# Optimization experiments

Hardware: AMD Instinct MI355X
Metric: run time of the kernel (lower is better)

## Reference

```python
import jax, jax.numpy as jnp
import numpy as np

T = 2048           # tokens (single prefill sequence)
HIDDEN = 2048
H = 16             # num heads
D_NOPE = 128
D_ROPE = 64
D_V = 128
KV_LORA = 512
EPS = 1e-6
ROPE_THETA = 10000.0


def setup_inputs() -> dict:
    key = jax.random.key(0)
    ks = jax.random.split(key, 7)
    s = 0.02
    return {
        "positions": jnp.arange(T, dtype=jnp.int64) if jax.config.jax_enable_x64 else jnp.arange(T, dtype=jnp.int32),
        "hidden_states": jax.random.normal(ks[0], (T, HIDDEN), dtype=jnp.float32),
        "w_q": jax.random.normal(ks[1], (HIDDEN, H * (D_NOPE + D_ROPE)), dtype=jnp.float32) * s,
        "w_kv_a": jax.random.normal(ks[2], (HIDDEN, KV_LORA + D_ROPE), dtype=jnp.float32) * s,
        "kv_a_ln_w": jax.random.uniform(ks[3], (KV_LORA,), dtype=jnp.float32, minval=0.5, maxval=1.5),
        "w_kv_b": jax.random.normal(ks[4], (KV_LORA, H * (D_NOPE + D_V)), dtype=jnp.float32) * s,
        "w_o": jax.random.normal(ks[5], (H * D_V, HIDDEN), dtype=jnp.float32) * s,
    }


def _rms_norm(x, w):
    var = jnp.mean(jnp.square(x), axis=-1, keepdims=True)
    return x * jax.lax.rsqrt(var + EPS) * w


def _rope_nonneox(x, positions):
    # x: [..., D_ROPE], GPT-J (interleaved) style rotation
    inv_freq = 1.0 / (ROPE_THETA ** (jnp.arange(0, D_ROPE, 2, dtype=jnp.float32) / D_ROPE))
    freqs = positions.astype(jnp.float32)[:, None] * inv_freq  # [T, D_ROPE//2]
    cos, sin = jnp.cos(freqs), jnp.sin(freqs)
    # broadcast over head dim if present
    while cos.ndim < x.ndim:
        cos, sin = cos[:, None], sin[:, None]
    x1, x2 = x[..., 0::2], x[..., 1::2]
    o1 = x1 * cos - x2 * sin
    o2 = x2 * cos + x1 * sin
    return jnp.stack([o1, o2], axis=-1).reshape(x.shape)


def reference(positions, hidden_states, w_q, w_kv_a, kv_a_ln_w, w_kv_b, w_o):
    scaling = (D_NOPE + D_ROPE) ** -0.5
    # q projection (q_lora_rank is None branch)
    q = (hidden_states @ w_q).reshape(T, H, D_NOPE + D_ROPE)
    q_nope, q_pe = q[..., :D_NOPE], q[..., D_NOPE:]
    # compressed KV latent
    latent = hidden_states @ w_kv_a                 # [T, KV_LORA + D_ROPE]
    kv_a = _rms_norm(latent[:, :KV_LORA], kv_a_ln_w)
    k_pe = latent[:, KV_LORA:]                      # [T, D_ROPE], shared across heads
    # decompress to per-head k_nope and v (kv_b_proj)
    kv = (kv_a @ w_kv_b).reshape(T, H, D_NOPE + D_V)
    k_nope, v = kv[..., :D_NOPE], kv[..., D_NOPE:]
    # non-neox RoPE
    q_pe = _rope_nonneox(q_pe, positions)
    k_pe = _rope_nonneox(k_pe, positions)           # [T, D_ROPE]
    # concat rope parts (k_pe broadcast over heads)
    q_full = jnp.concatenate([q_nope, q_pe], axis=-1)                         # [T,H,192]
    k_full = jnp.concatenate([k_nope, jnp.broadcast_to(k_pe[:, None, :], (T, H, D_ROPE))], axis=-1)
    # causal MHA
    scores = jnp.einsum("qhd,khd->hqk", q_full, k_full) * scaling
    causal = positions[:, None] >= positions[None, :]
    scores = jnp.where(causal[None], scores, -jnp.inf)
    attn = jax.nn.softmax(scores, axis=-1)
    out = jnp.einsum("hqk,khd->qhd", attn, v).reshape(T, H * D_V)
    return out @ w_o
```

## Files before the change

### kernel.cpp

```cpp
#include <hip/hip_runtime.h>
#include <hip/hip_bf16.h>
#include <stdint.h>

#define T_SEQ   2048
#define NHEAD   16
#define NPAD1   3712

typedef short bf16x8  __attribute__((ext_vector_type(8)));
typedef float f32x4   __attribute__((ext_vector_type(4)));
typedef float f32x16  __attribute__((ext_vector_type(16)));

__device__ __forceinline__ unsigned short f2bf(float f) {
  union { float f; uint32_t u; } v; v.f = f;
  uint32_t u = v.u;
  uint32_t r = u + 0x7FFF + ((u >> 16) & 1);
  return (unsigned short)(r >> 16);
}

__device__ __forceinline__ void async16(const void* g, void* l) {
  __builtin_amdgcn_global_load_lds(
      (const __attribute__((address_space(1))) void*)g,
      (__attribute__((address_space(3))) void*)l, 16, 0, 0);
}

__device__ __forceinline__ void tr32(const float* __restrict__ in,
    unsigned short* __restrict__ out, int R, int C, int bx, int by,
    float (*tile)[33], int tid) {
  int r0 = bx * 32, c0 = by * 32;
  int tx = tid & 31, ty = tid >> 5;
  for (int i = 0; i < 4; i++)
    tile[ty + i * 8][tx] = in[(size_t)(r0 + ty + i * 8) * C + c0 + tx];
  __syncthreads();
  for (int i = 0; i < 4; i++) {
    int c = ty + i * 8;
    out[(size_t)(c0 + c) * R + r0 + tx] = f2bf(tile[tx][c]);
  }
}

__global__ __launch_bounds__(256) void prep_kernel(
    const float* __restrict__ hs, const float* __restrict__ w_q,
    const float* __restrict__ w_kv_a, const float* __restrict__ w_kv_b,
    const float* __restrict__ w_o,
    unsigned short* __restrict__ hs_bf, unsigned short* __restrict__ wcat_t,
    unsigned short* __restrict__ wkvb_t, unsigned short* __restrict__ wo_t) {
  __shared__ float tile[32][33];
  int bid = blockIdx.x, tid = threadIdx.x;
  if (bid < 4096) {
    int i = (bid * 256 + tid) * 4;
    float4 v = *(const float4*)(hs + i);
    ushort4 o; o.x = f2bf(v.x); o.y = f2bf(v.y); o.z = f2bf(v.z); o.w = f2bf(v.w);
    *(ushort4*)(hs_bf + i) = o;
  } else if (bid < 4096 + 6144) {
    int l = bid - 4096;
    tr32(w_q, wcat_t, 2048, 3072, l & 63, l >> 6, tile, tid);
  } else if (bid < 4096 + 6144 + 1152) {
    int l = bid - (4096 + 6144);
    tr32(w_kv_a, wcat_t + (size_t)3072 * 2048, 2048, 576, l & 63, l >> 6, tile, tid);
  } else if (bid < 4096 + 6144 + 1152 + 2048) {
    int l = bid - (4096 + 6144 + 1152);
    tr32(w_kv_b, wkvb_t, 512, 4096, l & 15, l >> 4, tile, tid);
  } else if (bid < 4096 + 6144 + 1152 + 2048 + 4096) {
    int l = bid - (4096 + 6144 + 1152 + 2048);
    tr32(w_o, wo_t, 2048, 2048, l & 63, l >> 6, tile, tid);
  } else {
    int l = bid - (4096 + 6144 + 1152 + 2048 + 4096);
    uint4 z = (uint4){0, 0, 0, 0};
    *(uint4*)(wcat_t + (size_t)3648 * 2048 + (size_t)(l * 256 + tid) * 8) = z;
  }
}

template<int TM, int OUT_BF16>
__global__ __launch_bounds__(256) void gemm_bt_kernel(
    const unsigned short* __restrict__ A, const unsigned short* __restrict__ B,
    void* __restrict__ Cv, int M, int N, int K) {
  constexpr int MT = TM / 32;
  __shared__ __align__(16) unsigned short Asm[4][TM * 32];
  __shared__ __align__(16) unsigned short Bsm[4][128 * 32];
  int tid = threadIdx.x, wid = tid >> 6, lane = tid & 63;
  int lrow = lane & 15, lquad = lane >> 4;
  int cswz = (lquad ^ ((lane >> 1) & 3)) * 8;
  int m0 = blockIdx.x * TM, n0 = blockIdx.y * 128;
  int wm = (wid & 1) * (TM / 2), wn = (wid >> 1) * 64;

  int row_s = tid >> 2;
  int cc_s = (tid & 3) ^ ((tid >> 3) & 3);
  const unsigned short* Ag0 = A + (size_t)(m0 + row_s) * K + cc_s * 8;
  const unsigned short* Ag1 = A + (size_t)(m0 + row_s + 64) * K + cc_s * 8;
  const unsigned short* Bg0 = B + (size_t)(n0 + row_s) * K + cc_s * 8;
  const unsigned short* Bg1 = B + (size_t)(n0 + row_s + 64) * K + cc_s * 8;

  f32x4 acc[MT][4];
  for (int i = 0; i < MT; i++) for (int j = 0; j < 4; j++) acc[i][j] = (f32x4){0.f,0.f,0.f,0.f};

  auto stage = [&](int t, int buf) {
    int kk = t * 32;
    async16(Ag0 + kk, &Asm[buf][tid * 8]);
    if constexpr (TM == 128) async16(Ag1 + kk, &Asm[buf][2048 + tid * 8]);
    async16(Bg0 + kk, &Bsm[buf][tid * 8]);
    async16(Bg1 + kk, &Bsm[buf][2048 + tid * 8]);
  };

  const int ktiles = K >> 5;
  stage(0, 0); stage(1, 1); stage(2, 2);
  if constexpr (TM == 128) asm volatile("s_waitcnt vmcnt(8)" ::: "memory");
  else                     asm volatile("s_waitcnt vmcnt(6)" ::: "memory");
  __builtin_amdgcn_s_barrier();
  __builtin_amdgcn_sched_barrier(0);

  for (int t = 0; t < ktiles; ++t) {
    if (t + 3 < ktiles) stage(t + 3, (t + 3) & 3);
    __builtin_amdgcn_sched_barrier(0);
    const unsigned short* As = Asm[t & 3];
    const unsigned short* Bs = Bsm[t & 3];
    bf16x8 af[MT], bfr[4];
    for (int mt = 0; mt < MT; mt++)
      af[mt] = *(const bf16x8*)(As + (wm + mt * 16 + lrow) * 32 + cswz);
    for (int nf = 0; nf < 4; nf++)
      bfr[nf] = *(const bf16x8*)(Bs + (wn + nf * 16 + lrow) * 32 + cswz);
    for (int mt = 0; mt < MT; mt++)
      for (int nf = 0; nf < 4; nf++)
        acc[mt][nf] = __builtin_amdgcn_mfma_f32_16x16x32_bf16(af[mt], bfr[nf], acc[mt][nf], 0, 0, 0);
    __builtin_amdgcn_sched_barrier(0);
    if (t + 3 < ktiles) {
      if constexpr (TM == 128) asm volatile("s_waitcnt vmcnt(8)" ::: "memory");
      else                     asm volatile("s_waitcnt vmcnt(6)" ::: "memory");
    } else if (t + 2 < ktiles) {
      if constexpr (TM == 128) asm volatile("s_waitcnt vmcnt(4)" ::: "memory");
      else                     asm volatile("s_waitcnt vmcnt(3)" ::: "memory");
    } else if (t + 1 < ktiles) {
      asm volatile("s_waitcnt vmcnt(0)" ::: "memory");
    }
    __builtin_amdgcn_s_barrier();
    __builtin_amdgcn_sched_barrier(0);
  }

  for (int mt = 0; mt < MT; mt++)
    for (int nf = 0; nf < 4; nf++) {
      int row = m0 + wm + mt * 16 + lquad * 4;
      int col = n0 + wn + nf * 16 + lrow;
      for (int r = 0; r < 4; r++) {
        if (OUT_BF16)
          ((unsigned short*)Cv)[(size_t)(row + r) * N + col] = f2bf(acc[mt][nf][r]);
        else
          ((float*)Cv)[(size_t)(row + r) * N + col] = acc[mt][nf][r];
      }
    }
}

__global__ __launch_bounds__(256) void postproc1_kernel(
    const float* __restrict__ q_lat,
    const float* __restrict__ ln_w,
    const int* __restrict__ positions,
    unsigned short* __restrict__ kv_a,
    unsigned short* __restrict__ q_full,
    unsigned short* __restrict__ k_pe)
{
  int t = blockIdx.x, tid = threadIdx.x;
  const float* row = q_lat + (size_t)t * NPAD1;
  const float scaling = 0.07216878364870323f;

  float v0 = row[3072 + tid], v1 = row[3072 + 256 + tid];
  float ss = v0 * v0 + v1 * v1;
  for (int m = 1; m < 64; m <<= 1) ss += __shfl_xor(ss, m, 64);
  __shared__ float red[4];
  if ((tid & 63) == 0) red[tid >> 6] = ss;
  __shared__ float kro[64], cf[32], sf[32];
  float pos = (float)positions[t];
  if (tid < 32) {
    float inv_freq = powf(10000.f, -(float)(2 * tid) / 64.f);
    float c, s; sincosf(pos * inv_freq, &s, &c);
    cf[tid] = c; sf[tid] = s;
    float x1 = row[3584 + 2 * tid], x2 = row[3584 + 2 * tid + 1];
    kro[2 * tid]     = x1 * c - x2 * s;
    kro[2 * tid + 1] = x2 * c + x1 * s;
  }
  __syncthreads();
  float rstd = rsqrtf((red[0] + red[1] + red[2] + red[3]) * (1.f / 512.f) + 1e-6f);
  kv_a[(size_t)t * 512 + tid]       = f2bf(v0 * rstd * ln_w[tid]);
  kv_a[(size_t)t * 512 + 256 + tid] = f2bf(v1 * rstd * ln_w[256 + tid]);
  if (tid < 64) k_pe[(size_t)t * 64 + tid] = f2bf(kro[tid]);

  for (int i = tid; i < NHEAD * 128; i += 256) {
    int h = i >> 7, d = i & 127;
    q_full[((size_t)h * T_SEQ + t) * 192 + d] = f2bf(row[h * 192 + d] * scaling);
  }
  for (int i = tid; i < NHEAD * 32; i += 256) {
    int h = i >> 5, p = i & 31;
    float c = cf[p], s = sf[p];
    float x1 = row[h * 192 + 128 + 2 * p], x2 = row[h * 192 + 128 + 2 * p + 1];
    q_full[((size_t)h * T_SEQ + t) * 192 + 128 + 2 * p]     = f2bf((x1 * c - x2 * s) * scaling);
    q_full[((size_t)h * T_SEQ + t) * 192 + 128 + 2 * p + 1] = f2bf((x2 * c + x1 * s) * scaling);
  }
}

__global__ __launch_bounds__(256) void kvpost_kernel(
    const unsigned short* __restrict__ kv_b,
    const unsigned short* __restrict__ k_pe,
    unsigned short* __restrict__ k_full,
    unsigned short* __restrict__ v_t) {
  __shared__ unsigned short tile[32][41];
  int bid = blockIdx.x, tid = threadIdx.x;
  if (bid < 3072) {
    int idx = bid * 256 + tid;
    int cc = idx % 24, rest = idx / 24;
    int t = rest & (T_SEQ - 1), h = rest >> 11;
    uint4 v = (cc < 16)
        ? *(const uint4*)(kv_b + (size_t)t * 4096 + h * 256 + cc * 8)
        : *(const uint4*)(k_pe + (size_t)t * 64 + (cc - 16) * 8);
    *(uint4*)(k_full + (size_t)idx * 8) = v;
  } else {
    int l = bid - 3072;
    int h = l >> 8, t0 = (l & 63) * 32, d0 = ((l >> 6) & 3) * 32;
    int tx = tid & 31, ty = tid >> 5;
    for (int i = 0; i < 4; i++)
      tile[ty + i * 8][tx] = kv_b[(size_t)(t0 + ty + i * 8) * 4096 + h * 256 + 128 + d0 + tx];
    __syncthreads();
    for (int i = 0; i < 4; i++)
      v_t[((size_t)h * 128 + d0 + ty + i * 8) * T_SEQ + t0 + tx] = tile[tx][ty + i * 8];
  }
}

#define PP 76
__global__ __launch_bounds__(256, 2) void flash_kernel(
    const unsigned short* __restrict__ q_full,
    const unsigned short* __restrict__ k_full,
    const unsigned short* __restrict__ v_t,
    unsigned short* __restrict__ attn_out)
{
  __shared__ __align__(16) unsigned short Ksm[2][1536 * 8];
  __shared__ __align__(16) unsigned short Vsm[1024 * 8];
  __shared__ __align__(16) unsigned short Psm[64 * PP];
  __shared__ float Lred[2][64];
  int h = blockIdx.x;
  int y = blockIdx.y;
  int qb = (y < 16) ? (31 - y) : (y - 16);
  int tid = threadIdx.x, wid = tid >> 6, lane = tid & 63;
  int l31 = lane & 31, l5 = lane >> 5, x7 = l31 & 7;
  int rq = wid & 1, kq = wid >> 1;

  const unsigned short* kh = k_full + (size_t)h * T_SEQ * 192;
  const unsigned short* vh = v_t    + (size_t)h * 128 * T_SEQ;

  int gK[6], gV[4];
  #pragma unroll
  for (int j = 0; j < 6; j++) {
    int s = tid + j * 256, row = s / 24, cm = s - row * 24;
    gK[j] = row * 192 + (cm ^ (row & 7)) * 8;
  }
  #pragma unroll
  for (int j = 0; j < 4; j++) {
    int s = tid + j * 256, d = s >> 3;
    gV[j] = d * T_SEQ + ((s & 7) ^ (d & 7)) * 8;
  }
  int kxo[12];
  #pragma unroll
  for (int kc = 0; kc < 12; kc++)
    kxo[kc] = (kq * 32 + l31) * 192 + ((kc * 2 + l5) ^ x7) * 8;
  int vxb[2];
  #pragma unroll
  for (int ntv = 0; ntv < 2; ntv++) vxb[ntv] = (kq * 64 + ntv * 32 + l31) * 64;

  bf16x8 qf[12];
  {
    const unsigned short* qrow =
        q_full + ((size_t)h * T_SEQ + qb * 64 + rq * 32 + l31) * 192 + l5 * 8;
    #pragma unroll
    for (int kc = 0; kc < 12; kc++) qf[kc] = *(const bf16x8*)(qrow + kc * 16);
  }
  f32x16 oacc[2];
  for (int i = 0; i < 2; i++) oacc[i] = (f32x16)(0.f);
  float lsum[16];
  #pragma unroll
  for (int r = 0; r < 16; r++) lsum[r] = 0.f;
  int rl[16];
  #pragma unroll
  for (int r = 0; r < 16; r++) rl[r] = (r & 3) + 8 * (r >> 2) + 4 * l5;

  #pragma unroll
  for (int j = 0; j < 6; j++) async16(kh + gK[j], &Ksm[0][(tid + j * 256) * 8]);

  int cur = 0;
  for (int kb = 0; kb <= qb; kb++) {
    __syncthreads();
    {
      const unsigned short* vb = vh + kb * 64;
      #pragma unroll
      for (int j = 0; j < 4; j++) async16(vb + gV[j], &Vsm[(tid + j * 256) * 8]);
    }
    const unsigned short* Ks = Ksm[cur];
    f32x16 sacc = (f32x16)(0.f);
    #pragma unroll
    for (int kc = 0; kc < 12; kc++) {
      bf16x8 kf = *(const bf16x8*)(Ks + kxo[kc]);
      sacc = __builtin_amdgcn_mfma_f32_32x32x16_bf16(qf[kc], kf, sacc, 0, 0, 0);
    }
    if (kb == qb) {
      int col_g = kb * 64 + kq * 32 + l31;
      int row_b = qb * 64 + rq * 32;
      #pragma unroll
      for (int r = 0; r < 16; r++)
        if (col_g > row_b + rl[r]) sacc[r] = -1e30f;
    }
    #pragma unroll
    for (int r = 0; r < 16; r++) {
      float p = __expf(sacc[r]);
      sacc[r] = p;
      lsum[r] += p;
    }
    #pragma unroll
    for (int r = 0; r < 16; r++)
      Psm[(rq * 32 + rl[r]) * PP + kq * 32 + l31] = f2bf(sacc[r]);
    __syncthreads();
    if (kb < qb) {
      const unsigned short* kb1 = kh + (size_t)(kb + 1) * 64 * 192;
      #pragma unroll
      for (int j = 0; j < 6; j++) async16(kb1 + gK[j], &Ksm[cur ^ 1][(tid + j * 256) * 8]);
    }
    #pragma unroll
    for (int kc = 0; kc < 4; kc++) {
      bf16x8 pf = *(const bf16x8*)(Psm + (rq * 32 + l31) * PP + kc * 16 + l5 * 8);
      #pragma unroll
      for (int ntv = 0; ntv < 2; ntv++) {
        bf16x8 vf = *(const bf16x8*)(Vsm + vxb[ntv] + ((kc * 2 + l5) ^ x7) * 8);
        oacc[ntv] = __builtin_amdgcn_mfma_f32_32x32x16_bf16(pf, vf, oacc[ntv], 0, 0, 0);
      }
    }
    cur ^= 1;
  }

  #pragma unroll
  for (int r = 0; r < 16; r++) {
    float s = lsum[r];
    s += __shfl_xor(s, 1, 64);
    s += __shfl_xor(s, 2, 64);
    s += __shfl_xor(s, 4, 64);
    s += __shfl_xor(s, 8, 64);
    s += __shfl_xor(s, 16, 64);
    lsum[r] = s;
  }
  if (l31 == 0)
    #pragma unroll
    for (int r = 0; r < 16; r++) Lred[kq][rq * 32 + rl[r]] = lsum[r];
  __syncthreads();
  #pragma unroll
  for (int r = 0; r < 16; r++) {
    int row_l = rq * 32 + rl[r];
    float inv = 1.f / (Lred[0][row_l] + Lred[1][row_l]);
    int row_g = qb * 64 + row_l;
    #pragma unroll
    for (int ntv = 0; ntv < 2; ntv++)
      attn_out[(size_t)row_g * 2048 + h * 128 + kq * 64 + ntv * 32 + l31] =
          f2bf(oacc[ntv][r] * inv);
  }
}

extern "C" void kernel_launch(void* const* d_in, const int* in_sizes, int n_in,
                              void* d_out, int out_size, void* d_ws, size_t ws_size,
                              hipStream_t stream) {
  const int*   positions = (const int*)d_in[0];
  const float* hs     = (const float*)d_in[1];
  const float* w_q    = (const float*)d_in[2];
  const float* w_kv_a = (const float*)d_in[3];
  const float* ln_w   = (const float*)d_in[4];
  const float* w_kv_b = (const float*)d_in[5];
  const float* w_o    = (const float*)d_in[6];
  float* out = (float*)d_out;

  char* ws = (char*)d_ws;
  size_t off = 0;
  auto alloc = [&](size_t bytes) { void* p = ws + off; off += (bytes + 255) & ~(size_t)255; return p; };
  unsigned short* hs_bf   = (unsigned short*)alloc((size_t)2048 * 2048 * 2);
  unsigned short* wcat_t  = (unsigned short*)alloc((size_t)NPAD1 * 2048 * 2);
  float*          q_lat   = (float*)alloc((size_t)2048 * NPAD1 * 4);
  unsigned short* kv_a_bf = (unsigned short*)alloc((size_t)2048 * 512 * 2);
  unsigned short* wkvb_t  = (unsigned short*)alloc((size_t)4096 * 512 * 2);
  unsigned short* kv_b    = (unsigned short*)alloc((size_t)2048 * 4096 * 2);
  unsigned short* q_full  = (unsigned short*)alloc((size_t)NHEAD * 2048 * 192 * 2);
  unsigned short* k_pe    = (unsigned short*)alloc((size_t)2048 * 64 * 2);
  unsigned short* k_full  = (unsigned short*)alloc((size_t)NHEAD * 2048 * 192 * 2);
  unsigned short* v_t     = (unsigned short*)alloc((size_t)NHEAD * 128 * 2048 * 2);
  unsigned short* attn_o  = (unsigned short*)alloc((size_t)2048 * 2048 * 2);
  unsigned short* wo_t    = (unsigned short*)alloc((size_t)2048 * 2048 * 2);

  prep_kernel<<<17600, 256, 0, stream>>>(hs, w_q, w_kv_a, w_kv_b, w_o,
                                         hs_bf, wcat_t, wkvb_t, wo_t);
  gemm_bt_kernel<128, 0><<<dim3(16, 29), 256, 0, stream>>>(hs_bf, wcat_t, q_lat, 2048, NPAD1, 2048);
  postproc1_kernel<<<2048, 256, 0, stream>>>(q_lat, ln_w, positions, kv_a_bf, q_full, k_pe);
  gemm_bt_kernel<128, 1><<<dim3(16, 32), 256, 0, stream>>>(kv_a_bf, wkvb_t, kv_b, 2048, 4096, 512);
  kvpost_kernel<<<7168, 256, 0, stream>>>(kv_b, k_pe, k_full, v_t);
  flash_kernel<<<dim3(16, 32), 256, 0, stream>>>(q_full, k_full, v_t, attn_o);
  gemm_bt_kernel<64, 0><<<dim3(32, 16), 256, 0, stream>>>(attn_o, wo_t, out, 2048, 2048, 2048);
}
```

Measured before the change: 284.7 us.

## Split-K the fused QKV-latent GEMM and cut GEMM pipeline to 3 stages

The first projection GEMM (2048x3712x2048) now runs as a two-way split-K, writing two fp32 partial outputs that the postprocessing kernel sums as it reads them. This doubles the grid from 464 to 928 blocks so the many CUs are better filled. Separately, the GEMM LDS ring buffer drops from four to three stages with a prefetch distance of two, which cuts shared memory use and may raise occupancy. The cost is an extra fp32 partial buffer to write and read back, and less latency hiding in every GEMM.

Result: slower. 290.7 us (+2.1%).

```diff
diff --git a/kernel.cpp b/kernel.cpp
--- a/kernel.cpp
+++ b/kernel.cpp
@@ -69,25 +69,33 @@
   }
 }
 
-template<int TM, int OUT_BF16>
+template<int TM, int OUT_BF16, int SPLITK>
 __global__ __launch_bounds__(256) void gemm_bt_kernel(
     const unsigned short* __restrict__ A, const unsigned short* __restrict__ B,
-    void* __restrict__ Cv, int M, int N, int K) {
+    void* __restrict__ Cv, int M, int N, int K, int ldk) {
   constexpr int MT = TM / 32;
-  __shared__ __align__(16) unsigned short Asm[4][TM * 32];
-  __shared__ __align__(16) unsigned short Bsm[4][128 * 32];
+  constexpr int LPS = (TM == 128) ? 4 : 3;
+  __shared__ __align__(16) unsigned short Asm[3][TM * 32];
+  __shared__ __align__(16) unsigned short Bsm[3][128 * 32];
   int tid = threadIdx.x, wid = tid >> 6, lane = tid & 63;
   int lrow = lane & 15, lquad = lane >> 4;
   int cswz = (lquad ^ ((lane >> 1) & 3)) * 8;
   int m0 = blockIdx.x * TM, n0 = blockIdx.y * 128;
   int wm = (wid & 1) * (TM / 2), wn = (wid >> 1) * 64;
 
+  if (SPLITK) {
+    int kz = blockIdx.z;
+    A += (size_t)kz * K;
+    B += (size_t)kz * K;
+    Cv = (void*)((float*)Cv + (size_t)blockIdx.z * M * N);
+  }
+
   int row_s = tid >> 2;
   int cc_s = (tid & 3) ^ ((tid >> 3) & 3);
-  const unsigned short* Ag0 = A + (size_t)(m0 + row_s) * K + cc_s * 8;
-  const unsigned short* Ag1 = A + (size_t)(m0 + row_s + 64) * K + cc_s * 8;
-  const unsigned short* Bg0 = B + (size_t)(n0 + row_s) * K + cc_s * 8;
-  const unsigned short* Bg1 = B + (size_t)(n0 + row_s + 64) * K + cc_s * 8;
+  const unsigned short* Ag0 = A + (size_t)(m0 + row_s) * ldk + cc_s * 8;
+  const unsigned short* Ag1 = A + (size_t)(m0 + row_s + 64) * ldk + cc_s * 8;
+  const unsigned short* Bg0 = B + (size_t)(n0 + row_s) * ldk + cc_s * 8;
+  const unsigned short* Bg1 = B + (size_t)(n0 + row_s + 64) * ldk + cc_s * 8;
 
   f32x4 acc[MT][4];
   for (int i = 0; i < MT; i++) for (int j = 0; j < 4; j++) acc[i][j] = (f32x4){0.f,0.f,0.f,0.f};
@@ -101,17 +109,18 @@
   };
 
   const int ktiles = K >> 5;
-  stage(0, 0); stage(1, 1); stage(2, 2);
-  if constexpr (TM == 128) asm volatile("s_waitcnt vmcnt(8)" ::: "memory");
-  else                     asm volatile("s_waitcnt vmcnt(6)" ::: "memory");
+  stage(0, 0); stage(1, 1);
+  if constexpr (TM == 128) asm volatile("s_waitcnt vmcnt(4)" ::: "memory");
+  else                     asm volatile("s_waitcnt vmcnt(3)" ::: "memory");
   __builtin_amdgcn_s_barrier();
   __builtin_amdgcn_sched_barrier(0);
 
+  int bc = 0, b2 = 2;
   for (int t = 0; t < ktiles; ++t) {
-    if (t + 3 < ktiles) stage(t + 3, (t + 3) & 3);
+    if (t + 2 < ktiles) stage(t + 2, b2);
     __builtin_amdgcn_sched_barrier(0);
-    const unsigned short* As = Asm[t & 3];
-    const unsigned short* Bs = Bsm[t & 3];
+    const unsigned short* As = Asm[bc];
+    const unsigned short* Bs = Bsm[bc];
     bf16x8 af[MT], bfr[4];
     for (int mt = 0; mt < MT; mt++)
       af[mt] = *(const bf16x8*)(As + (wm + mt * 16 + lrow) * 32 + cswz);
@@ -121,10 +130,7 @@
       for (int nf = 0; nf < 4; nf++)
         acc[mt][nf] = __builtin_amdgcn_mfma_f32_16x16x32_bf16(af[mt], bfr[nf], acc[mt][nf], 0, 0, 0);
     __builtin_amdgcn_sched_barrier(0);
-    if (t + 3 < ktiles) {
-      if constexpr (TM == 128) asm volatile("s_waitcnt vmcnt(8)" ::: "memory");
-      else                     asm volatile("s_waitcnt vmcnt(6)" ::: "memory");
-    } else if (t + 2 < ktiles) {
+    if (t + 2 < ktiles) {
       if constexpr (TM == 128) asm volatile("s_waitcnt vmcnt(4)" ::: "memory");
       else                     asm volatile("s_waitcnt vmcnt(3)" ::: "memory");
     } else if (t + 1 < ktiles) {
@@ -132,6 +138,8 @@
     }
     __builtin_amdgcn_s_barrier();
     __builtin_amdgcn_sched_barrier(0);
+    bc = (bc == 2) ? 0 : bc + 1;
+    b2 = (b2 == 2) ? 0 : b2 + 1;
   }
 
   for (int mt = 0; mt < MT; mt++)
@@ -156,10 +164,12 @@
     unsigned short* __restrict__ k_pe)
 {
   int t = blockIdx.x, tid = threadIdx.x;
-  const float* row = q_lat + (size_t)t * NPAD1;
+  const float* row  = q_lat + (size_t)t * NPAD1;
+  const float* row2 = row + (size_t)T_SEQ * NPAD1;
   const float scaling = 0.07216878364870323f;
 
-  float v0 = row[3072 + tid], v1 = row[3072 + 256 + tid];
+  float v0 = row[3072 + tid] + row2[3072 + tid];
+  float v1 = row[3072 + 256 + tid] + row2[3072 + 256 + tid];
   float ss = v0 * v0 + v1 * v1;
   for (int m = 1; m < 64; m <<= 1) ss += __shfl_xor(ss, m, 64);
   __shared__ float red[4];
@@ -170,7 +180,8 @@
     float inv_freq = powf(10000.f, -(float)(2 * tid) / 64.f);
     float c, s; sincosf(pos * inv_freq, &s, &c);
     cf[tid] = c; sf[tid] = s;
-    float x1 = row[3584 + 2 * tid], x2 = row[3584 + 2 * tid + 1];
+    float x1 = row[3584 + 2 * tid] + row2[3584 + 2 * tid];
+    float x2 = row[3584 + 2 * tid + 1] + row2[3584 + 2 * tid + 1];
     kro[2 * tid]     = x1 * c - x2 * s;
     kro[2 * tid + 1] = x2 * c + x1 * s;
   }
@@ -182,12 +193,14 @@
 
   for (int i = tid; i < NHEAD * 128; i += 256) {
     int h = i >> 7, d = i & 127;
-    q_full[((size_t)h * T_SEQ + t) * 192 + d] = f2bf(row[h * 192 + d] * scaling);
+    float q = row[h * 192 + d] + row2[h * 192 + d];
+    q_full[((size_t)h * T_SEQ + t) * 192 + d] = f2bf(q * scaling);
   }
   for (int i = tid; i < NHEAD * 32; i += 256) {
     int h = i >> 5, p = i & 31;
     float c = cf[p], s = sf[p];
-    float x1 = row[h * 192 + 128 + 2 * p], x2 = row[h * 192 + 128 + 2 * p + 1];
+    float x1 = row[h * 192 + 128 + 2 * p] + row2[h * 192 + 128 + 2 * p];
+    float x2 = row[h * 192 + 128 + 2 * p + 1] + row2[h * 192 + 128 + 2 * p + 1];
     q_full[((size_t)h * T_SEQ + t) * 192 + 128 + 2 * p]     = f2bf((x1 * c - x2 * s) * scaling);
     q_full[((size_t)h * T_SEQ + t) * 192 + 128 + 2 * p + 1] = f2bf((x2 * c + x1 * s) * scaling);
   }
@@ -371,7 +384,7 @@
   auto alloc = [&](size_t bytes) { void* p = ws + off; off += (bytes + 255) & ~(size_t)255; return p; };
   unsigned short* hs_bf   = (unsigned short*)alloc((size_t)2048 * 2048 * 2);
   unsigned short* wcat_t  = (unsigned short*)alloc((size_t)NPAD1 * 2048 * 2);
-  float*          q_lat   = (float*)alloc((size_t)2048 * NPAD1 * 4);
+  float*          q_lat   = (float*)alloc((size_t)2 * 2048 * NPAD1 * 4);
   unsigned short* kv_a_bf = (unsigned short*)alloc((size_t)2048 * 512 * 2);
   unsigned short* wkvb_t  = (unsigned short*)alloc((size_t)4096 * 512 * 2);
   unsigned short* kv_b    = (unsigned short*)alloc((size_t)2048 * 4096 * 2);
@@ -384,10 +397,10 @@
 
   prep_kernel<<<17600, 256, 0, stream>>>(hs, w_q, w_kv_a, w_kv_b, w_o,
                                          hs_bf, wcat_t, wkvb_t, wo_t);
-  gemm_bt_kernel<128, 0><<<dim3(16, 29), 256, 0, stream>>>(hs_bf, wcat_t, q_lat, 2048, NPAD1, 2048);
+  gemm_bt_kernel<128, 0, 1><<<dim3(16, 29, 2), 256, 0, stream>>>(hs_bf, wcat_t, q_lat, 2048, NPAD1, 1024, 2048);
   postproc1_kernel<<<2048, 256, 0, stream>>>(q_lat, ln_w, positions, kv_a_bf, q_full, k_pe);
-  gemm_bt_kernel<128, 1><<<dim3(16, 32), 256, 0, stream>>>(kv_a_bf, wkvb_t, kv_b, 2048, 4096, 512);
+  gemm_bt_kernel<128, 1, 0><<<dim3(16, 32), 256, 0, stream>>>(kv_a_bf, wkvb_t, kv_b, 2048, 4096, 512, 512);
   kvpost_kernel<<<7168, 256, 0, stream>>>(kv_b, k_pe, k_full, v_t);
   flash_kernel<<<dim3(16, 32), 256, 0, stream>>>(q_full, k_full, v_t, attn_o);
-  gemm_bt_kernel<64, 0><<<dim3(32, 16), 256, 0, stream>>>(attn_o, wo_t, out, 2048, 2048, 2048);
-}
+  gemm_bt_kernel<64, 0, 0><<<dim3(32, 16), 256, 0, stream>>>(attn_o, wo_t, out, 2048, 2048, 2048, 2048);
+}
```
